# Kernel tuning notes

Hardware: AMD Instinct MI355X
Metric: run time of the kernel (lower is better)

## Reference

```python
import jax, jax.numpy as jnp
import numpy as np

LN_EPS = 1e-5   # torch LayerNorm default
EPS = 1e-8      # slot-attention renorm eps
ITERS = 3


def _ln(x, g, b):
    m = jnp.mean(x, axis=-1, keepdims=True)
    v = jnp.mean(jnp.square(x - m), axis=-1, keepdims=True)
    return (x - m) * jax.lax.rsqrt(v + LN_EPS) * g + b


def _gru(x, h, W_ih, W_hh, b_ih, b_hh):
    # torch GRUCell: gates ordered r, z, n; weight_* has shape [3h, in]
    gi = x @ W_ih.T + b_ih
    gh = h @ W_hh.T + b_hh
    ir, iz, inn = jnp.split(gi, 3, axis=-1)
    hr, hz, hn = jnp.split(gh, 3, axis=-1)
    r = jax.nn.sigmoid(ir + hr)
    z = jax.nn.sigmoid(iz + hz)
    n = jnp.tanh(inn + r * hn)
    return (1.0 - z) * n + z * h


def setup_inputs() -> dict:
    key = jax.random.key(0)
    ks = jax.random.split(key, 16)
    b, n, d, n_s = 32, 4096, 256, 8
    h = max(d, 128)  # hidden_dim = max(dim, hidden_dim)
    s = 1.0 / np.sqrt(d)
    inp = {
        "inputs": jax.random.normal(ks[0], (b, n, d), jnp.float32),
        "noise": jax.random.normal(ks[1], (b, n_s, d), jnp.float32),
        "slots_mu": jax.random.normal(ks[2], (1, 1, d), jnp.float32),
        "slots_logsigma": jax.random.normal(ks[3], (1, 1, d), jnp.float32) * 0.1,
        "Wq": jax.random.uniform(ks[4], (d, d), jnp.float32, -s, s),
        "bq": jnp.zeros((d,), jnp.float32),
        "Wk": jax.random.uniform(ks[5], (d, d), jnp.float32, -s, s),
        "bk": jnp.zeros((d,), jnp.float32),
        "Wv": jax.random.uniform(ks[6], (d, d), jnp.float32, -s, s),
        "bv": jnp.zeros((d,), jnp.float32),
        "W_ih": jax.random.uniform(ks[7], (3 * d, d), jnp.float32, -s, s),
        "W_hh": jax.random.uniform(ks[8], (3 * d, d), jnp.float32, -s, s),
        "b_ih": jnp.zeros((3 * d,), jnp.float32),
        "b_hh": jnp.zeros((3 * d,), jnp.float32),
        "W1": jax.random.uniform(ks[9], (h, d), jnp.float32, -s, s),
        "b1": jnp.zeros((h,), jnp.float32),
        "W2": jax.random.uniform(ks[10], (d, h), jnp.float32, -s, s),
        "b2": jnp.zeros((d,), jnp.float32),
        "g_in": jnp.ones((d,), jnp.float32), "be_in": jnp.zeros((d,), jnp.float32),
        "g_sl": jnp.ones((d,), jnp.float32), "be_sl": jnp.zeros((d,), jnp.float32),
        "g_ff": jnp.ones((d,), jnp.float32), "be_ff": jnp.zeros((d,), jnp.float32),
    }
    return inp


def reference(inputs, noise, slots_mu, slots_logsigma, Wq, bq, Wk, bk, Wv, bv,
              W_ih, W_hh, b_ih, b_hh, W1, b1, W2, b2,
              g_in, be_in, g_sl, be_sl, g_ff, be_ff):
    b, n, d = inputs.shape
    scale = d ** (-0.5)
    # reparameterized slot init
    slots = slots_mu + jnp.exp(slots_logsigma) * noise          # [b, n_s, d]
    x = _ln(inputs, g_in, be_in)
    k = x @ Wk.T + bk                                           # [b, n, d]
    v = x @ Wv.T + bv
    attn = None
    for _ in range(ITERS):
        slots_prev = slots
        q = _ln(slots, g_sl, be_sl) @ Wq.T + bq                 # [b, n_s, d]
        dots = jnp.einsum('bid,bjd->bij', q, k) * scale         # [b, n_s, n]
        attn = jax.nn.softmax(dots, axis=1)                     # softmax over SLOTS
        attn_ = attn + EPS
        attn_ = attn_ / jnp.sum(attn_, axis=-1, keepdims=True)  # renorm over inputs
        updates = jnp.einsum('bjd,bij->bid', v, attn_)          # [b, n_s, d]
        slots = _gru(updates.reshape(-1, d), slots_prev.reshape(-1, d),
                     W_ih, W_hh, b_ih, b_hh).reshape(b, -1, d)
        pre = _ln(slots, g_ff, be_ff)
        slots = slots + (jax.nn.relu(pre @ W1.T + b1) @ W2.T + b2)
    return (slots, attn)
```

## Files before the change

kernel.cpp:

```cpp
#include <hip/hip_runtime.h>
#include <hip/hip_fp16.h>
#include <cstdint>
#include <cstddef>


#define NTOK 4096
#define DDIM 256
#define NSLOT 8
#define NBATCH 32
#define CH 64
#define NCHK 64
#define SROWS (NBATCH * NSLOT)
#define NROWS (NBATCH * NTOK)
#define SCALE 0.0625f
#define LN_EPS_C 1e-5f
#define ATTN_EPS_C 1e-8f

__device__ __forceinline__ void wave_reduce2(float& s, float& ss) {
#pragma unroll
  for (int off = 32; off > 0; off >>= 1) {
    s  += __shfl_down(s, off, 64);
    ss += __shfl_down(ss, off, 64);
  }
}
__device__ __forceinline__ void wave_reduce2_xor(float& s, float& ss) {
#pragma unroll
  for (int off = 32; off > 0; off >>= 1) {
    s  += __shfl_xor(s, off, 64);
    ss += __shfl_xor(ss, off, 64);
  }
}

__global__ __launch_bounds__(256) void convert_weights_k(
    const float* __restrict__ Wq, const float* __restrict__ Wv,
    const float* __restrict__ Wih, const float* __restrict__ Whh,
    const float* __restrict__ W1, const float* __restrict__ W2,
    const float* __restrict__ Wk, __half* __restrict__ WqT,
    __half* __restrict__ WvT, __half* __restrict__ WihT,
    __half* __restrict__ WhhT, __half* __restrict__ W1T,
    __half* __restrict__ W2T, __half* __restrict__ Wk_h) {
  __shared__ float tile[32][33];
  int bz = blockIdx.x;
  int tx = threadIdx.x & 31, ty = threadIdx.x >> 5;
  if (bz >= 80) {
    int ro = (bz - 80) * 32, cd = blockIdx.y * 32;
#pragma unroll
    for (int p = 0; p < 32; p += 8)
      Wk_h[(size_t)(ro + ty + p) * DDIM + cd + tx] =
          __float2half(Wk[(size_t)(ro + ty + p) * DDIM + cd + tx]);
    return;
  }
  const float* in; __half* out; int O, bo;
  if (bz < 8)       { in = Wq;  out = WqT;  O = 256; bo = bz; }
  else if (bz < 16) { in = Wv;  out = WvT;  O = 256; bo = bz - 8; }
  else if (bz < 40) { in = Wih; out = WihT; O = 768; bo = bz - 16; }
  else if (bz < 64) { in = Whh; out = WhhT; O = 768; bo = bz - 40; }
  else if (bz < 72) { in = W1;  out = W1T;  O = 256; bo = bz - 64; }
  else              { in = W2;  out = W2T;  O = 256; bo = bz - 72; }
  int ro = bo * 32, cd = blockIdx.y * 32;
#pragma unroll
  for (int p = 0; p < 32; p += 8)
    tile[ty + p][tx] = in[(size_t)(ro + ty + p) * DDIM + cd + tx];
  __syncthreads();
#pragma unroll
  for (int p = 0; p < 32; p += 8)
    out[(size_t)(cd + ty + p) * O + ro + tx] = __float2half(tile[tx][ty + p]);
}

__global__ __launch_bounds__(256) void xh_prep_k(
    const float* __restrict__ X, const float* __restrict__ g,
    const float* __restrict__ be, __half* __restrict__ xh) {
  int row = blockIdx.x * 4 + (threadIdx.x >> 6);
  int lane = threadIdx.x & 63;
  float4 a = *(const float4*)(X + (size_t)row * DDIM + lane * 4);
  float s = a.x + a.y + a.z + a.w;
  float ss = a.x * a.x + a.y * a.y + a.z * a.z + a.w * a.w;
  wave_reduce2_xor(s, ss);
  float m = s * (1.f / DDIM);
  float rs = rsqrtf(ss * (1.f / DDIM) - m * m + LN_EPS_C);
  float4 gv = *(const float4*)(g + lane * 4);
  float4 bev = *(const float4*)(be + lane * 4);
  union { __half2 h[2]; uint2 u; } pk;
  pk.h[0] = __floats2half2_rn((a.x - m) * rs * gv.x + bev.x,
                              (a.y - m) * rs * gv.y + bev.y);
  pk.h[1] = __floats2half2_rn((a.z - m) * rs * gv.z + bev.z,
                              (a.w - m) * rs * gv.w + bev.w);
  *(uint2*)(xh + (size_t)row * DDIM + lane * 4) = pk.u;
}

__global__ __launch_bounds__(256) void fused_attn_f16_k(
    const __half* __restrict__ xh, const float* __restrict__ qk,
    const float* __restrict__ qkb, float* __restrict__ attn_out,
    float* __restrict__ S_part, __half* __restrict__ u_part, int write_attn) {
  __shared__ __half sx[CH][258];
  __shared__ float4 sq4[NSLOT][64];
  __shared__ float part[4][NSLOT][CH];
  __shared__ float sa[NSLOT][CH];
  __shared__ float sC0[NSLOT], sS[NSLOT];
  int b = blockIdx.x, c = blockIdx.y, t = threadIdx.x;
#pragma unroll
  for (int r2 = 0; r2 < 2; ++r2) {
    int idx = r2 * 256 + t;
    int i = idx >> 6, quad = idx & 63;
    sq4[i][quad] = *(const float4*)(qk + ((size_t)b * NSLOT + i) * DDIM + quad * 4);
  }
  if (t < NSLOT) sC0[t] = qkb[b * NSLOT + t];
  const size_t base = (size_t)b * NTOK + (size_t)c * CH;
#pragma unroll
  for (int it = 0; it < 8; ++it) {
    int e = it * 256 + t;
    int row = e >> 5, c16 = e & 31;
    uint4 v = *(const uint4*)(xh + (base + row) * DDIM + c16 * 8);
    __half2* dst = (__half2*)&sx[row][c16 * 8];
    dst[0] = ((const __half2*)&v)[0];
    dst[1] = ((const __half2*)&v)[1];
    dst[2] = ((const __half2*)&v)[2];
    dst[3] = ((const __half2*)&v)[3];
  }
  __syncthreads();
  {
    int tj = t & 31, qd = t >> 5;
    float2 xa[16], xb[16];
    const __half2* xra = (const __half2*)&sx[tj][qd * 32];
    const __half2* xrb = (const __half2*)&sx[tj + 32][qd * 32];
#pragma unroll
    for (int d2 = 0; d2 < 16; ++d2) {
      xa[d2] = __half22float2(xra[d2]);
      xb[d2] = __half22float2(xrb[d2]);
    }
    int w = t >> 6;
    bool lo = (t & 63) < 32;
#pragma unroll
    for (int i = 0; i < NSLOT; ++i) {
      float pa = 0.f, pb = 0.f;
#pragma unroll
      for (int d4 = 0; d4 < 8; ++d4) {
        float4 q = sq4[i][qd * 8 + d4];
        pa = fmaf(xa[2 * d4].x, q.x, fmaf(xa[2 * d4].y, q.y,
             fmaf(xa[2 * d4 + 1].x, q.z, fmaf(xa[2 * d4 + 1].y, q.w, pa))));
        pb = fmaf(xb[2 * d4].x, q.x, fmaf(xb[2 * d4].y, q.y,
             fmaf(xb[2 * d4 + 1].x, q.z, fmaf(xb[2 * d4 + 1].y, q.w, pb))));
      }
      pa += __shfl_down(pa, 32, 64);
      pb += __shfl_down(pb, 32, 64);
      if (lo) { part[w][i][tj] = pa; part[w][i][tj + 32] = pb; }
    }
  }
  __syncthreads();
  if (t < CH) {
    float dots[NSLOT], mx = -1e30f;
#pragma unroll
    for (int i = 0; i < NSLOT; ++i) {
      dots[i] = part[0][i][t] + part[1][i][t] + part[2][i][t] +
                part[3][i][t] + sC0[i];
      mx = fmaxf(mx, dots[i]);
    }
    float sum = 0.f;
#pragma unroll
    for (int i = 0; i < NSLOT; ++i) { dots[i] = expf(dots[i] - mx); sum += dots[i]; }
    float inv = 1.f / sum;
#pragma unroll
    for (int i = 0; i < NSLOT; ++i) {
      float a = dots[i] * inv;
      if (write_attn)
        attn_out[((size_t)b * NSLOT + i) * NTOK + c * CH + t] = a;
      float ae = a + ATTN_EPS_C;
      sa[i][t] = ae;
      float ps = ae;
#pragma unroll
      for (int off = 32; off > 0; off >>= 1) ps += __shfl_down(ps, off, 64);
      if (t == 0) sS[i] = ps;
    }
  }
  __syncthreads();
  float acc[NSLOT] = {};
#pragma unroll
  for (int jj = 0; jj < CH; ++jj) {
    float x = __half2float(sx[jj][t]);
#pragma unroll
    for (int i = 0; i < NSLOT; ++i) acc[i] = fmaf(x, sa[i][jj], acc[i]);
  }
  __half* upb = u_part + (((size_t)b * NCHK + c) * NSLOT) * DDIM + t;
#pragma unroll
  for (int i = 0; i < NSLOT; ++i) upb[(size_t)i * DDIM] = __float2half(acc[i]);
  if (t < NSLOT) S_part[((size_t)b * NCHK + c) * NSLOT + t] = sS[t];
}

__global__ __launch_bounds__(1024) void slot_update_k(
    const __half* __restrict__ u_part, const float* __restrict__ S_part,
    const float* __restrict__ slots_in, const __half* __restrict__ WvT,
    const float* __restrict__ bv, const __half* __restrict__ WihT,
    const __half* __restrict__ WhhT, const float* __restrict__ b_ih,
    const float* __restrict__ b_hh, const float* __restrict__ g_ff,
    const float* __restrict__ be_ff, const __half* __restrict__ W1T,
    const float* __restrict__ b1, const __half* __restrict__ W2T,
    const float* __restrict__ b2, const float* __restrict__ g_sl,
    const float* __restrict__ be_sl, const __half* __restrict__ WqT,
    const float* __restrict__ bq, const __half* __restrict__ Wk_h,
    const float* __restrict__ bk, const float* __restrict__ noise,
    const float* __restrict__ mu, const float* __restrict__ logsig,
    float* __restrict__ slots_out, float* __restrict__ qk,
    float* __restrict__ qkb_out, int init, int compute_qk) {
  __shared__ float red[4][6][DDIM];
  __shared__ float su[DDIM], sh[DDIM], supd[DDIM], v1[DDIM], v2[DDIM];
  __shared__ float scal[16];
  int r = blockIdx.x, t = threadIdx.x;
  int b = r >> 3, i = r & 7;
  int o = t & 255, ks = t >> 8;
  int lane = t & 63, wid = t >> 6;
  if (init) {
    if (ks == 0) {
      float ns = mu[o] + expf(logsig[o]) * noise[(size_t)r * DDIM + o];
      slots_out[(size_t)r * DDIM + o] = ns;
      v2[o] = ns;
    }
    __syncthreads();
  } else {
    {
      float up = 0.f;
      const __half* upp =
          u_part + (((size_t)b * NCHK + ks * 16) * NSLOT + i) * DDIM + o;
#pragma unroll
      for (int cc = 0; cc < 16; ++cc)
        up += __half2float(upp[(size_t)cc * (NSLOT * DDIM)]);
      red[ks][0][o] = up;
    }
    if (t < 64) {
      float sp = S_part[((size_t)b * NCHK + t) * NSLOT + i];
#pragma unroll
      for (int off = 32; off > 0; off >>= 1) sp += __shfl_down(sp, off, 64);
      if (t == 0) scal[0] = sp;
    }
    if (ks == 0) sh[o] = slots_in[(size_t)r * DDIM + o];
    __syncthreads();
    if (ks == 0) {
      float invS = 1.f / scal[0];
      su[o] = (red[0][0][o] + red[1][0][o] + red[2][0][o] + red[3][0][o]) * invS;
    }
    __syncthreads();
    {
      float p = 0.f;
      const __half* wp = WvT + (size_t)(ks * 64) * DDIM + o;
#pragma unroll 8
      for (int dd = 0; dd < 64; ++dd)
        p = fmaf(su[ks * 64 + dd], __half2float(wp[(size_t)dd * DDIM]), p);
      red[ks][0][o] = p;
    }
    __syncthreads();
    if (ks == 0)
      supd[o] = bv[o] + red[0][0][o] + red[1][0][o] + red[2][0][o] + red[3][0][o];
    __syncthreads();
    {
      float p0 = 0, p1 = 0, p2 = 0, p3 = 0, p4 = 0, p5 = 0;
      const __half* pi = WihT + (size_t)(ks * 64) * (3 * DDIM) + o;
      const __half* ph = WhhT + (size_t)(ks * 64) * (3 * DDIM) + o;
#pragma unroll 4
      for (int dd = 0; dd < 64; ++dd) {
        float ud = supd[ks * 64 + dd], hd = sh[ks * 64 + dd];
        size_t off = (size_t)dd * (3 * DDIM);
        p0 = fmaf(ud, __half2float(pi[off]), p0);
        p1 = fmaf(ud, __half2float(pi[off + DDIM]), p1);
        p2 = fmaf(ud, __half2float(pi[off + 2 * DDIM]), p2);
        p3 = fmaf(hd, __half2float(ph[off]), p3);
        p4 = fmaf(hd, __half2float(ph[off + DDIM]), p4);
        p5 = fmaf(hd, __half2float(ph[off + 2 * DDIM]), p5);
      }
      red[ks][0][o] = p0; red[ks][1][o] = p1; red[ks][2][o] = p2;
      red[ks][3][o] = p3; red[ks][4][o] = p4; red[ks][5][o] = p5;
    }
    __syncthreads();
    if (ks == 0) {
      float air = b_ih[o] + red[0][0][o] + red[1][0][o] + red[2][0][o] + red[3][0][o];
      float aiz = b_ih[DDIM + o] + red[0][1][o] + red[1][1][o] + red[2][1][o] + red[3][1][o];
      float ain = b_ih[2 * DDIM + o] + red[0][2][o] + red[1][2][o] + red[2][2][o] + red[3][2][o];
      float ahr = b_hh[o] + red[0][3][o] + red[1][3][o] + red[2][3][o] + red[3][3][o];
      float ahz = b_hh[DDIM + o] + red[0][4][o] + red[1][4][o] + red[2][4][o] + red[3][4][o];
      float ahn = b_hh[2 * DDIM + o] + red[0][5][o] + red[1][5][o] + red[2][5][o] + red[3][5][o];
      float rg = 1.f / (1.f + expf(-(air + ahr)));
      float zg = 1.f / (1.f + expf(-(aiz + ahz)));
      float ng = tanhf(ain + rg * ahn);
      float nh = (1.f - zg) * ng + zg * sh[o];
      v1[o] = nh;
      float s2 = nh, ss2 = nh * nh;
      wave_reduce2(s2, ss2);
      if (lane == 0) { scal[wid] = s2; scal[4 + wid] = ss2; }
    }
    __syncthreads();
    if (ks == 0) {
      float sS = scal[0] + scal[1] + scal[2] + scal[3];
      float sQ = scal[4] + scal[5] + scal[6] + scal[7];
      float m = sS * (1.f / DDIM);
      float rs = rsqrtf(sQ * (1.f / DDIM) - m * m + LN_EPS_C);
      v2[o] = (v1[o] - m) * rs * g_ff[o] + be_ff[o];
    }
    __syncthreads();
    {
      float p = 0.f;
      const __half* wp = W1T + (size_t)(ks * 64) * DDIM + o;
#pragma unroll 8
      for (int dd = 0; dd < 64; ++dd)
        p = fmaf(v2[ks * 64 + dd], __half2float(wp[(size_t)dd * DDIM]), p);
      red[ks][0][o] = p;
    }
    __syncthreads();
    if (ks == 0)
      su[o] = fmaxf(b1[o] + red[0][0][o] + red[1][0][o] + red[2][0][o] + red[3][0][o], 0.f);
    __syncthreads();
    {
      float p = 0.f;
      const __half* wp = W2T + (size_t)(ks * 64) * DDIM + o;
#pragma unroll 8
      for (int dd = 0; dd < 64; ++dd)
        p = fmaf(su[ks * 64 + dd], __half2float(wp[(size_t)dd * DDIM]), p);
      red[ks][0][o] = p;
    }
    __syncthreads();
    if (ks == 0) {
      float out = v1[o] + b2[o] + red[0][0][o] + red[1][0][o] + red[2][0][o] + red[3][0][o];
      slots_out[(size_t)r * DDIM + o] = out;
      v2[o] = out;
    }
    __syncthreads();
  }
  if (!compute_qk) return;
  if (ks == 0) {
    float x = v2[o];
    float s2 = x, ss2 = x * x;
    wave_reduce2(s2, ss2);
    if (lane == 0) { scal[wid] = s2; scal[4 + wid] = ss2; }
  }
  __syncthreads();
  if (ks == 0) {
    float sS = scal[0] + scal[1] + scal[2] + scal[3];
    float sQ = scal[4] + scal[5] + scal[6] + scal[7];
    float m = sS * (1.f / DDIM);
    float rs = rsqrtf(sQ * (1.f / DDIM) - m * m + LN_EPS_C);
    su[o] = (v2[o] - m) * rs * g_sl[o] + be_sl[o];
  }
  __syncthreads();
  {
    float p = 0.f;
    const __half* wp = WqT + (size_t)(ks * 64) * DDIM + o;
#pragma unroll 8
    for (int dd = 0; dd < 64; ++dd)
      p = fmaf(su[ks * 64 + dd], __half2float(wp[(size_t)dd * DDIM]), p);
    red[ks][0][o] = p;
  }
  __syncthreads();
  if (ks == 0)
    sh[o] = bq[o] + red[0][0][o] + red[1][0][o] + red[2][0][o] + red[3][0][o];
  __syncthreads();
  {
    float p = 0.f;
    const __half* wp = Wk_h + (size_t)(ks * 64) * DDIM + o;
#pragma unroll 8
    for (int dd = 0; dd < 64; ++dd)
      p = fmaf(sh[ks * 64 + dd], __half2float(wp[(size_t)dd * DDIM]), p);
    red[ks][0][o] = p;
  }
  __syncthreads();
  if (ks == 0) {
    float qkv = SCALE * (red[0][0][o] + red[1][0][o] + red[2][0][o] + red[3][0][o]);
    qk[(size_t)r * DDIM + o] = qkv;
    float v0 = sh[o] * bk[o], d1 = 0.f;
    wave_reduce2(v0, d1);
    if (lane == 0) scal[wid] = v0;
  }
  __syncthreads();
  if (t == 0)
    qkb_out[r] = SCALE * (scal[0] + scal[1] + scal[2] + scal[3]);
}

extern "C" void kernel_launch(void* const* d_in, const int* in_sizes, int n_in,
                              void* d_out, int out_size, void* d_ws,
                              size_t ws_size, hipStream_t stream) {
  const float* inputs   = (const float*)d_in[0];
  const float* noise    = (const float*)d_in[1];
  const float* slots_mu = (const float*)d_in[2];
  const float* slots_ls = (const float*)d_in[3];
  const float* Wq   = (const float*)d_in[4];
  const float* bq   = (const float*)d_in[5];
  const float* Wk   = (const float*)d_in[6];
  const float* bk   = (const float*)d_in[7];
  const float* Wv   = (const float*)d_in[8];
  const float* bv   = (const float*)d_in[9];
  const float* W_ih = (const float*)d_in[10];
  const float* W_hh = (const float*)d_in[11];
  const float* b_ih = (const float*)d_in[12];
  const float* b_hh = (const float*)d_in[13];
  const float* W1   = (const float*)d_in[14];
  const float* b1   = (const float*)d_in[15];
  const float* W2   = (const float*)d_in[16];
  const float* b2   = (const float*)d_in[17];
  const float* g_in = (const float*)d_in[18];
  const float* be_in= (const float*)d_in[19];
  const float* g_sl = (const float*)d_in[20];
  const float* be_sl= (const float*)d_in[21];
  const float* g_ff = (const float*)d_in[22];
  const float* be_ff= (const float*)d_in[23];

  float* out_slots = (float*)d_out;
  float* out_attn  = (float*)d_out + SROWS * DDIM;

  float* w = (float*)d_ws;
  float* slots = w;  w += SROWS * DDIM;
  float* qk = w;     w += SROWS * DDIM;
  float* qkb = w;    w += SROWS;
  float* S_part = w; w += NBATCH * NCHK * NSLOT;
  __half* h = (__half*)w;
  __half* xh = h;     h += (size_t)NROWS * DDIM;
  __half* u_part = h; h += (size_t)NBATCH * NCHK * NSLOT * DDIM;
  __half* WqT_h = h;  h += DDIM * DDIM;
  __half* WvT_h = h;  h += DDIM * DDIM;
  __half* WihT_h = h; h += DDIM * 3 * DDIM;
  __half* WhhT_h = h; h += DDIM * 3 * DDIM;
  __half* W1T_h = h;  h += DDIM * DDIM;
  __half* W2T_h = h;  h += DDIM * DDIM;
  __half* Wk_h = h;   h += DDIM * DDIM;

  convert_weights_k<<<dim3(88, 8), 256, 0, stream>>>(
      Wq, Wv, W_ih, W_hh, W1, W2, Wk, WqT_h, WvT_h, WihT_h, WhhT_h, W1T_h,
      W2T_h, Wk_h);
  slot_update_k<<<SROWS, 1024, 0, stream>>>(
      u_part, S_part, slots, WvT_h, bv, WihT_h, WhhT_h, b_ih, b_hh, g_ff,
      be_ff, W1T_h, b1, W2T_h, b2, g_sl, be_sl, WqT_h, bq, Wk_h, bk, noise,
      slots_mu, slots_ls, slots, qk, qkb, 1, 1);
  xh_prep_k<<<NROWS / 4, 256, 0, stream>>>(inputs, g_in, be_in, xh);
  for (int it = 0; it < 3; ++it) {
    fused_attn_f16_k<<<dim3(NBATCH, NCHK), 256, 0, stream>>>(
        xh, qk, qkb, out_attn, S_part, u_part, (it == 2) ? 1 : 0);
    float* sout = (it == 2) ? out_slots : slots;
    slot_update_k<<<SROWS, 1024, 0, stream>>>(
        u_part, S_part, slots, WvT_h, bv, WihT_h, WhhT_h, b_ih, b_hh, g_ff,
        be_ff, W1T_h, b1, W2T_h, b2, g_sl, be_sl, WqT_h, bq, Wk_h, bk, noise,
        slots_mu, slots_ls, sout, qk, qkb, 0, (it == 2) ? 0 : 1);
  }
}
```

Baseline: 240.6 us.

## Double-buffer token chunks via async global-to-LDS loads in fused attention

Each attention block now processes four token chunks instead of one, loading chunks with global_load_lds into two XOR-swizzled LDS buffers so the next chunk's load overlaps the current chunk's compute. The query is stored in LDS as half2, and the renormalised attention reuses the partial-sum buffer. The goal is to hide global load latency, cut LDS bank conflicts and amortise per-block setup. The grid shrinks fourfold, which lowers parallelism, and the hand-placed waitcnt and barrier ordering is fragile.

```diff
diff --git a/kernel.cpp b/kernel.cpp
--- a/kernel.cpp
+++ b/kernel.cpp
@@ -92,98 +92,143 @@
     const __half* __restrict__ xh, const float* __restrict__ qk,
     const float* __restrict__ qkb, float* __restrict__ attn_out,
     float* __restrict__ S_part, __half* __restrict__ u_part, int write_attn) {
-  __shared__ __half sx[CH][258];
-  __shared__ float4 sq4[NSLOT][64];
+  __shared__ __align__(16) char sx[2][CH * 512];
+  __shared__ __half2 sqh[NSLOT][128];
   __shared__ float part[4][NSLOT][CH];
-  __shared__ float sa[NSLOT][CH];
-  __shared__ float sC0[NSLOT], sS[NSLOT];
-  int b = blockIdx.x, c = blockIdx.y, t = threadIdx.x;
-#pragma unroll
-  for (int r2 = 0; r2 < 2; ++r2) {
+#define SA(i, j) part[0][i][j]
+  int b = blockIdx.x, t = threadIdx.x;
+  int c0 = blockIdx.y * 4;
+  int lane = t & 63, w = t >> 6;
+
+#pragma unroll
+  for (int r2 = 0; r2 < 4; ++r2) {
     int idx = r2 * 256 + t;
-    int i = idx >> 6, quad = idx & 63;
-    sq4[i][quad] = *(const float4*)(qk + ((size_t)b * NSLOT + i) * DDIM + quad * 4);
-  }
-  if (t < NSLOT) sC0[t] = qkb[b * NSLOT + t];
-  const size_t base = (size_t)b * NTOK + (size_t)c * CH;
-#pragma unroll
-  for (int it = 0; it < 8; ++it) {
-    int e = it * 256 + t;
-    int row = e >> 5, c16 = e & 31;
-    uint4 v = *(const uint4*)(xh + (base + row) * DDIM + c16 * 8);
-    __half2* dst = (__half2*)&sx[row][c16 * 8];
-    dst[0] = ((const __half2*)&v)[0];
-    dst[1] = ((const __half2*)&v)[1];
-    dst[2] = ((const __half2*)&v)[2];
-    dst[3] = ((const __half2*)&v)[3];
-  }
-  __syncthreads();
-  {
-    int tj = t & 31, qd = t >> 5;
-    float2 xa[16], xb[16];
-    const __half2* xra = (const __half2*)&sx[tj][qd * 32];
-    const __half2* xrb = (const __half2*)&sx[tj + 32][qd * 32];
-#pragma unroll
-    for (int d2 = 0; d2 < 16; ++d2) {
-      xa[d2] = __half22float2(xra[d2]);
-      xb[d2] = __half22float2(xrb[d2]);
-    }
-    int w = t >> 6;
-    bool lo = (t & 63) < 32;
-#pragma unroll
-    for (int i = 0; i < NSLOT; ++i) {
-      float pa = 0.f, pb = 0.f;
-#pragma unroll
-      for (int d4 = 0; d4 < 8; ++d4) {
-        float4 q = sq4[i][qd * 8 + d4];
-        pa = fmaf(xa[2 * d4].x, q.x, fmaf(xa[2 * d4].y, q.y,
-             fmaf(xa[2 * d4 + 1].x, q.z, fmaf(xa[2 * d4 + 1].y, q.w, pa))));
-        pb = fmaf(xb[2 * d4].x, q.x, fmaf(xb[2 * d4].y, q.y,
-             fmaf(xb[2 * d4 + 1].x, q.z, fmaf(xb[2 * d4 + 1].y, q.w, pb))));
-      }
-      pa += __shfl_down(pa, 32, 64);
-      pb += __shfl_down(pb, 32, 64);
-      if (lo) { part[w][i][tj] = pa; part[w][i][tj + 32] = pb; }
-    }
-  }
-  __syncthreads();
-  if (t < CH) {
-    float dots[NSLOT], mx = -1e30f;
-#pragma unroll
-    for (int i = 0; i < NSLOT; ++i) {
-      dots[i] = part[0][i][t] + part[1][i][t] + part[2][i][t] +
-                part[3][i][t] + sC0[i];
-      mx = fmaxf(mx, dots[i]);
-    }
-    float sum = 0.f;
-#pragma unroll
-    for (int i = 0; i < NSLOT; ++i) { dots[i] = expf(dots[i] - mx); sum += dots[i]; }
-    float inv = 1.f / sum;
-#pragma unroll
-    for (int i = 0; i < NSLOT; ++i) {
-      float a = dots[i] * inv;
-      if (write_attn)
-        attn_out[((size_t)b * NSLOT + i) * NTOK + c * CH + t] = a;
-      float ae = a + ATTN_EPS_C;
-      sa[i][t] = ae;
-      float ps = ae;
-#pragma unroll
-      for (int off = 32; off > 0; off >>= 1) ps += __shfl_down(ps, off, 64);
-      if (t == 0) sS[i] = ps;
-    }
-  }
-  __syncthreads();
-  float acc[NSLOT] = {};
-#pragma unroll
-  for (int jj = 0; jj < CH; ++jj) {
-    float x = __half2float(sx[jj][t]);
-#pragma unroll
-    for (int i = 0; i < NSLOT; ++i) acc[i] = fmaf(x, sa[i][jj], acc[i]);
-  }
-  __half* upb = u_part + (((size_t)b * NCHK + c) * NSLOT) * DDIM + t;
-#pragma unroll
-  for (int i = 0; i < NSLOT; ++i) upb[(size_t)i * DDIM] = __float2half(acc[i]);
-  if (t < NSLOT) S_part[((size_t)b * NCHK + c) * NSLOT + t] = sS[t];
+    int i = idx >> 7, d2 = idx & 127;
+    const float* qr = qk + ((size_t)b * NSLOT + i) * DDIM + d2 * 2;
+    sqh[i][d2] = __floats2half2_rn(qr[0], qr[1]);
+  }
+
+  const size_t rowb = (size_t)b * NTOK;
+
+  auto issue = [&](int buf, int chunk) {
+#pragma unroll
+    for (int k = 0; k < 8; ++k) {
+      int seg = w * 8 + k;
+      int L = (seg << 10) + lane * 16;
+      int row = L >> 9, col = L & 511;
+      int scol = col ^ ((row & 15) << 4);
+      const __half* src =
+          xh + (rowb + (size_t)chunk * CH + row) * DDIM + (scol >> 1);
+      __builtin_amdgcn_global_load_lds(
+          (const __attribute__((address_space(1))) void*)src,
+          (__attribute__((address_space(3))) void*)(&sx[buf][seg << 10]),
+          16, 0, 0);
+    }
+  };
+
+  auto compute = [&](int buf, int chunk) {
+    const char* sb = sx[buf];
+    {
+      int tj = t & 31, qd = (t >> 5) & 7;
+      int sw = (tj & 15) << 4;
+      float2 xa[16], xb[16];
+#pragma unroll
+      for (int d2 = 0; d2 < 16; ++d2) {
+        int ca = qd * 64 + d2 * 4;
+        xa[d2] = __half22float2(*(const __half2*)(sb + tj * 512 + (ca ^ sw)));
+        xb[d2] =
+            __half22float2(*(const __half2*)(sb + (tj + 32) * 512 + (ca ^ sw)));
+      }
+      bool lo = (t & 63) < 32;
+#pragma unroll
+      for (int i = 0; i < NSLOT; ++i) {
+        float pa = 0.f, pb = 0.f;
+#pragma unroll
+        for (int d2 = 0; d2 < 16; ++d2) {
+          float2 qf = __half22float2(sqh[i][qd * 16 + d2]);
+          pa = fmaf(xa[d2].x, qf.x, fmaf(xa[d2].y, qf.y, pa));
+          pb = fmaf(xb[d2].x, qf.x, fmaf(xb[d2].y, qf.y, pb));
+        }
+        pa += __shfl_down(pa, 32, 64);
+        pb += __shfl_down(pb, 32, 64);
+        if (lo) { part[w][i][tj] = pa; part[w][i][tj + 32] = pb; }
+      }
+    }
+    asm volatile("s_waitcnt lgkmcnt(0)" ::: "memory");
+    __builtin_amdgcn_s_barrier();
+    if (t < CH) {
+      float dots[NSLOT], mx = -1e30f;
+#pragma unroll
+      for (int i = 0; i < NSLOT; ++i) {
+        dots[i] = part[0][i][t] + part[1][i][t] + part[2][i][t] +
+                  part[3][i][t] + qkb[b * NSLOT + i];
+        mx = fmaxf(mx, dots[i]);
+      }
+      float sum = 0.f;
+#pragma unroll
+      for (int i = 0; i < NSLOT; ++i) {
+        dots[i] = expf(dots[i] - mx);
+        sum += dots[i];
+      }
+      float inv = 1.f / sum;
+#pragma unroll
+      for (int i = 0; i < NSLOT; ++i) {
+        float a = dots[i] * inv;
+        if (write_attn)
+          attn_out[((size_t)b * NSLOT + i) * NTOK + chunk * CH + t] = a;
+        dots[i] = a + ATTN_EPS_C;
+      }
+#pragma unroll
+      for (int i = 0; i < NSLOT; ++i) {
+        float ps = dots[i];
+#pragma unroll
+        for (int off = 32; off > 0; off >>= 1) ps += __shfl_down(ps, off, 64);
+        if (t == 0) S_part[((size_t)b * NCHK + chunk) * NSLOT + i] = ps;
+      }
+#pragma unroll
+      for (int i = 0; i < NSLOT; ++i) SA(i, t) = dots[i];
+    }
+    asm volatile("s_waitcnt lgkmcnt(0)" ::: "memory");
+    __builtin_amdgcn_s_barrier();
+    {
+      float acc[NSLOT] = {};
+#pragma unroll 8
+      for (int jj = 0; jj < CH; ++jj) {
+        int ad = jj * 512 + ((2 * t) ^ ((jj & 15) << 4));
+        float x = __half2float(*(const __half*)(sb + ad));
+#pragma unroll
+        for (int i = 0; i < NSLOT; ++i) acc[i] = fmaf(x, SA(i, jj), acc[i]);
+      }
+      __half* upb = u_part + (((size_t)b * NCHK + chunk) * NSLOT) * DDIM + t;
+#pragma unroll
+      for (int i = 0; i < NSLOT; ++i)
+        upb[(size_t)i * DDIM] = __float2half(acc[i]);
+    }
+  };
+
+  issue(0, c0);
+  issue(1, c0 + 1);
+  asm volatile("s_waitcnt vmcnt(8) lgkmcnt(0)" ::: "memory");
+  __builtin_amdgcn_s_barrier();
+  compute(0, c0);
+  asm volatile("s_waitcnt lgkmcnt(0)" ::: "memory");
+  __builtin_amdgcn_s_barrier();
+  issue(0, c0 + 2);
+  asm volatile("s_waitcnt vmcnt(8)" ::: "memory");
+  __builtin_amdgcn_s_barrier();
+  compute(1, c0 + 1);
+  asm volatile("s_waitcnt lgkmcnt(0)" ::: "memory");
+  __builtin_amdgcn_s_barrier();
+  issue(1, c0 + 3);
+  asm volatile("s_waitcnt vmcnt(8)" ::: "memory");
+  __builtin_amdgcn_s_barrier();
+  compute(0, c0 + 2);
+  asm volatile("s_waitcnt lgkmcnt(0)" ::: "memory");
+  __builtin_amdgcn_s_barrier();
+  asm volatile("s_waitcnt vmcnt(0)" ::: "memory");
+  __builtin_amdgcn_s_barrier();
+  compute(1, c0 + 3);
+#undef SA
 }
 
 __global__ __launch_bounds__(1024) void slot_update_k(
@@ -427,7 +472,7 @@
       slots_mu, slots_ls, slots, qk, qkb, 1, 1);
   xh_prep_k<<<NROWS / 4, 256, 0, stream>>>(inputs, g_in, be_in, xh);
   for (int it = 0; it < 3; ++it) {
-    fused_attn_f16_k<<<dim3(NBATCH, NCHK), 256, 0, stream>>>(
+    fused_attn_f16_k<<<dim3(NBATCH, 16), 256, 0, stream>>>(
         xh, qk, qkb, out_attn, S_part, u_part, (it == 2) ? 1 : 0);
     float* sout = (it == 2) ? out_slots : slots;
     slot_update_k<<<SROWS, 1024, 0, stream>>>(
```

Result: slower. 280.4 us (+16.6%).

## Split fused attention into packed-f16 dot/softmax kernel and separate update kernel

Applied to the files above, without the earlier changes.

Replaces the single fused attention kernel with two kernels. The first computes slot dots with packed f16 `fdot2` against register-resident q, does the softmax over slots, writes eps-shifted attention weights to global memory as half, and emits per-chunk sums. The second rereads xh to accumulate weighted updates over 256-token chunks and writes the attn output from the stored half weights. This drops the shared-memory staging and cross-wave reductions, at the cost of reading xh twice per iteration and storing the final attention at reduced precision.

```diff
diff --git a/kernel.cpp b/kernel.cpp
--- a/kernel.cpp
+++ b/kernel.cpp
@@ -8,13 +8,19 @@
 #define DDIM 256
 #define NSLOT 8
 #define NBATCH 32
-#define CH 64
-#define NCHK 64
 #define SROWS (NBATCH * NSLOT)
 #define NROWS (NBATCH * NTOK)
 #define SCALE 0.0625f
 #define LN_EPS_C 1e-5f
 #define ATTN_EPS_C 1e-8f
+
+typedef _Float16 f16x2 __attribute__((ext_vector_type(2)));
+
+__device__ __forceinline__ f16x2 u2h(unsigned u) {
+  union { unsigned u; f16x2 h; } c;
+  c.u = u;
+  return c.h;
+}
 
 __device__ __forceinline__ void wave_reduce2(float& s, float& ss) {
 #pragma unroll
@@ -88,102 +94,115 @@
   *(uint2*)(xh + (size_t)row * DDIM + lane * 4) = pk.u;
 }
 
-__global__ __launch_bounds__(256) void fused_attn_f16_k(
+__global__ __launch_bounds__(256) void dots_k(
     const __half* __restrict__ xh, const float* __restrict__ qk,
-    const float* __restrict__ qkb, float* __restrict__ attn_out,
-    float* __restrict__ S_part, __half* __restrict__ u_part, int write_attn) {
-  __shared__ __half sx[CH][258];
-  __shared__ float4 sq4[NSLOT][64];
-  __shared__ float part[4][NSLOT][CH];
-  __shared__ float sa[NSLOT][CH];
-  __shared__ float sC0[NSLOT], sS[NSLOT];
-  int b = blockIdx.x, c = blockIdx.y, t = threadIdx.x;
-#pragma unroll
-  for (int r2 = 0; r2 < 2; ++r2) {
-    int idx = r2 * 256 + t;
-    int i = idx >> 6, quad = idx & 63;
-    sq4[i][quad] = *(const float4*)(qk + ((size_t)b * NSLOT + i) * DDIM + quad * 4);
-  }
-  if (t < NSLOT) sC0[t] = qkb[b * NSLOT + t];
-  const size_t base = (size_t)b * NTOK + (size_t)c * CH;
-#pragma unroll
+    const float* __restrict__ qkb, __half* __restrict__ ae_g,
+    float* __restrict__ S_part) {
+  __shared__ float red[4][8];
+  int b = blockIdx.x, g = blockIdx.y, t = threadIdx.x;
+  int w = t >> 6, lane = t & 63;
+  int sub = lane >> 4, r = lane & 15;
+  f16x2 qk2[NSLOT][8];
+#pragma unroll
+  for (int i = 0; i < NSLOT; ++i) {
+    const float* qr = qk + ((size_t)b * NSLOT + i) * DDIM + r * 16;
+#pragma unroll
+    for (int d4 = 0; d4 < 4; ++d4) {
+      float4 q4 = *(const float4*)(qr + d4 * 4);
+      qk2[i][d4 * 2] = (f16x2){(_Float16)q4.x, (_Float16)q4.y};
+      qk2[i][d4 * 2 + 1] = (f16x2){(_Float16)q4.z, (_Float16)q4.w};
+    }
+  }
+  float qkb_r[NSLOT];
+#pragma unroll
+  for (int i = 0; i < NSLOT; ++i) qkb_r[i] = qkb[b * NSLOT + i];
+  float sacc = 0.f;
+  const size_t tokbase = (size_t)b * NTOK + (size_t)g * 128;
   for (int it = 0; it < 8; ++it) {
-    int e = it * 256 + t;
-    int row = e >> 5, c16 = e & 31;
-    uint4 v = *(const uint4*)(xh + (base + row) * DDIM + c16 * 8);
-    __half2* dst = (__half2*)&sx[row][c16 * 8];
-    dst[0] = ((const __half2*)&v)[0];
-    dst[1] = ((const __half2*)&v)[1];
-    dst[2] = ((const __half2*)&v)[2];
-    dst[3] = ((const __half2*)&v)[3];
-  }
-  __syncthreads();
-  {
-    int tj = t & 31, qd = t >> 5;
-    float2 xa[16], xb[16];
-    const __half2* xra = (const __half2*)&sx[tj][qd * 32];
-    const __half2* xrb = (const __half2*)&sx[tj + 32][qd * 32];
-#pragma unroll
-    for (int d2 = 0; d2 < 16; ++d2) {
-      xa[d2] = __half22float2(xra[d2]);
-      xb[d2] = __half22float2(xrb[d2]);
-    }
-    int w = t >> 6;
-    bool lo = (t & 63) < 32;
+    int tok = it * 16 + w * 4 + sub;
+    const __half* xr = xh + (tokbase + tok) * DDIM + r * 16;
+    uint4 v0 = *(const uint4*)(xr);
+    uint4 v1 = *(const uint4*)(xr + 8);
+    f16x2 x2[8];
+    x2[0] = u2h(v0.x); x2[1] = u2h(v0.y); x2[2] = u2h(v0.z); x2[3] = u2h(v0.w);
+    x2[4] = u2h(v1.x); x2[5] = u2h(v1.y); x2[6] = u2h(v1.z); x2[7] = u2h(v1.w);
+    float p[NSLOT];
 #pragma unroll
     for (int i = 0; i < NSLOT; ++i) {
-      float pa = 0.f, pb = 0.f;
-#pragma unroll
-      for (int d4 = 0; d4 < 8; ++d4) {
-        float4 q = sq4[i][qd * 8 + d4];
-        pa = fmaf(xa[2 * d4].x, q.x, fmaf(xa[2 * d4].y, q.y,
-             fmaf(xa[2 * d4 + 1].x, q.z, fmaf(xa[2 * d4 + 1].y, q.w, pa))));
-        pb = fmaf(xb[2 * d4].x, q.x, fmaf(xb[2 * d4].y, q.y,
-             fmaf(xb[2 * d4 + 1].x, q.z, fmaf(xb[2 * d4 + 1].y, q.w, pb))));
-      }
-      pa += __shfl_down(pa, 32, 64);
-      pb += __shfl_down(pb, 32, 64);
-      if (lo) { part[w][i][tj] = pa; part[w][i][tj + 32] = pb; }
-    }
-  }
-  __syncthreads();
-  if (t < CH) {
-    float dots[NSLOT], mx = -1e30f;
+      float s = 0.f;
+#pragma unroll
+      for (int d2 = 0; d2 < 8; ++d2)
+        s = __builtin_amdgcn_fdot2(x2[d2], qk2[i][d2], s, false);
+      p[i] = s;
+    }
 #pragma unroll
     for (int i = 0; i < NSLOT; ++i) {
-      dots[i] = part[0][i][t] + part[1][i][t] + part[2][i][t] +
-                part[3][i][t] + sC0[i];
-      mx = fmaxf(mx, dots[i]);
-    }
+      p[i] += __shfl_xor(p[i], 1, 64);
+      p[i] += __shfl_xor(p[i], 2, 64);
+      p[i] += __shfl_xor(p[i], 4, 64);
+      p[i] += __shfl_xor(p[i], 8, 64);
+      p[i] += qkb_r[i];
+    }
+    float mx = -1e30f;
+#pragma unroll
+    for (int i = 0; i < NSLOT; ++i) mx = fmaxf(mx, p[i]);
     float sum = 0.f;
 #pragma unroll
-    for (int i = 0; i < NSLOT; ++i) { dots[i] = expf(dots[i] - mx); sum += dots[i]; }
+    for (int i = 0; i < NSLOT; ++i) { p[i] = expf(p[i] - mx); sum += p[i]; }
     float inv = 1.f / sum;
-#pragma unroll
-    for (int i = 0; i < NSLOT; ++i) {
-      float a = dots[i] * inv;
-      if (write_attn)
-        attn_out[((size_t)b * NSLOT + i) * NTOK + c * CH + t] = a;
-      float ae = a + ATTN_EPS_C;
-      sa[i][t] = ae;
-      float ps = ae;
-#pragma unroll
-      for (int off = 32; off > 0; off >>= 1) ps += __shfl_down(ps, off, 64);
-      if (t == 0) sS[i] = ps;
-    }
-  }
+    if (r < NSLOT) {
+      float ae = p[r] * inv + ATTN_EPS_C;
+      ae_g[(tokbase + tok) * NSLOT + r] = __float2half(ae);
+      sacc += ae;
+    }
+  }
+  sacc += __shfl_down(sacc, 32, 64);
+  sacc += __shfl_down(sacc, 16, 64);
+  if (lane < NSLOT) red[w][lane] = sacc;
+  __syncthreads();
+  if (t < NSLOT) {
+    float s = red[0][t] + red[1][t] + red[2][t] + red[3][t];
+    S_part[((size_t)b * 32 + g) * NSLOT + t] = s;
+  }
+}
+
+__global__ __launch_bounds__(256) void update_k(
+    const __half* __restrict__ xh, const __half* __restrict__ ae_g,
+    float* __restrict__ attn_out, __half* __restrict__ u_part,
+    int write_attn) {
+  __shared__ __align__(16) __half sa[256 * NSLOT];
+  int b = blockIdx.x, g = blockIdx.y, t = threadIdx.x;
+  const size_t tokbase = (size_t)b * NTOK + (size_t)g * 256;
+  *(uint4*)&sa[t * 8] = *(const uint4*)(ae_g + tokbase * NSLOT + t * 8);
   __syncthreads();
   float acc[NSLOT] = {};
-#pragma unroll
-  for (int jj = 0; jj < CH; ++jj) {
-    float x = __half2float(sx[jj][t]);
-#pragma unroll
-    for (int i = 0; i < NSLOT; ++i) acc[i] = fmaf(x, sa[i][jj], acc[i]);
-  }
-  __half* upb = u_part + (((size_t)b * NCHK + c) * NSLOT) * DDIM + t;
+  const __half* xb = xh + tokbase * DDIM + t;
+#pragma unroll 8
+  for (int jj = 0; jj < 256; ++jj) {
+    float x = __half2float(xb[(size_t)jj * DDIM]);
+    const __half2* a2 = (const __half2*)&sa[jj * 8];
+    float2 f0 = __half22float2(a2[0]);
+    float2 f1 = __half22float2(a2[1]);
+    float2 f2 = __half22float2(a2[2]);
+    float2 f3 = __half22float2(a2[3]);
+    acc[0] = fmaf(x, f0.x, acc[0]);
+    acc[1] = fmaf(x, f0.y, acc[1]);
+    acc[2] = fmaf(x, f1.x, acc[2]);
+    acc[3] = fmaf(x, f1.y, acc[3]);
+    acc[4] = fmaf(x, f2.x, acc[4]);
+    acc[5] = fmaf(x, f2.y, acc[5]);
+    acc[6] = fmaf(x, f3.x, acc[6]);
+    acc[7] = fmaf(x, f3.y, acc[7]);
+  }
+  __half* upb = u_part + (((size_t)b * 16 + g) * NSLOT) * DDIM + t;
 #pragma unroll
   for (int i = 0; i < NSLOT; ++i) upb[(size_t)i * DDIM] = __float2half(acc[i]);
-  if (t < NSLOT) S_part[((size_t)b * NCHK + c) * NSLOT + t] = sS[t];
+  if (write_attn) {
+#pragma unroll
+    for (int i = 0; i < NSLOT; ++i)
+      attn_out[((size_t)b * NSLOT + i) * NTOK + g * 256 + t] =
+          __half2float(sa[t * 8 + i]) - ATTN_EPS_C;
+  }
 }
 
 __global__ __launch_bounds__(1024) void slot_update_k(
@@ -219,16 +238,16 @@
     {
       float up = 0.f;
       const __half* upp =
-          u_part + (((size_t)b * NCHK + ks * 16) * NSLOT + i) * DDIM + o;
-#pragma unroll
-      for (int cc = 0; cc < 16; ++cc)
+          u_part + (((size_t)b * 16 + ks * 4) * NSLOT + i) * DDIM + o;
+#pragma unroll
+      for (int cc = 0; cc < 4; ++cc)
         up += __half2float(upp[(size_t)cc * (NSLOT * DDIM)]);
       red[ks][0][o] = up;
     }
     if (t < 64) {
-      float sp = S_part[((size_t)b * NCHK + t) * NSLOT + i];
-#pragma unroll
-      for (int off = 32; off > 0; off >>= 1) sp += __shfl_down(sp, off, 64);
+      float sp = (t < 32) ? S_part[((size_t)b * 32 + t) * NSLOT + i] : 0.f;
+#pragma unroll
+      for (int off = 16; off > 0; off >>= 1) sp += __shfl_down(sp, off, 64);
       if (t == 0) scal[0] = sp;
     }
     if (ks == 0) sh[o] = slots_in[(size_t)r * DDIM + o];
@@ -406,10 +425,11 @@
   float* slots = w;  w += SROWS * DDIM;
   float* qk = w;     w += SROWS * DDIM;
   float* qkb = w;    w += SROWS;
-  float* S_part = w; w += NBATCH * NCHK * NSLOT;
+  float* S_part = w; w += NBATCH * 32 * NSLOT;
   __half* h = (__half*)w;
   __half* xh = h;     h += (size_t)NROWS * DDIM;
-  __half* u_part = h; h += (size_t)NBATCH * NCHK * NSLOT * DDIM;
+  __half* u_part = h; h += (size_t)NBATCH * 16 * NSLOT * DDIM;
+  __half* ae_g = h;   h += (size_t)NROWS * NSLOT;
   __half* WqT_h = h;  h += DDIM * DDIM;
   __half* WvT_h = h;  h += DDIM * DDIM;
   __half* WihT_h = h; h += DDIM * 3 * DDIM;
@@ -427,8 +447,9 @@
       slots_mu, slots_ls, slots, qk, qkb, 1, 1);
   xh_prep_k<<<NROWS / 4, 256, 0, stream>>>(inputs, g_in, be_in, xh);
   for (int it = 0; it < 3; ++it) {
-    fused_attn_f16_k<<<dim3(NBATCH, NCHK), 256, 0, stream>>>(
-        xh, qk, qkb, out_attn, S_part, u_part, (it == 2) ? 1 : 0);
+    dots_k<<<dim3(NBATCH, 32), 256, 0, stream>>>(xh, qk, qkb, ae_g, S_part);
+    update_k<<<dim3(NBATCH, 16), 256, 0, stream>>>(
+        xh, ae_g, out_attn, u_part, (it == 2) ? 1 : 0);
     float* sout = (it == 2) ? out_slots : slots;
     slot_update_k<<<SROWS, 1024, 0, stream>>>(
         u_part, S_part, slots, WvT_h, bv, WihT_h, WhhT_h, b_ih, b_hh, g_ff,
```

Measured after the change: 270.1 us. 12.3% more time.

## Restructure attention kernel to per-wave register streaming with fdot2 and deferred attn transpose

Applied to the files above, without the earlier changes.

The shared-memory tiled attention kernel is replaced by a wave-per-64-token design. Each half-wave streams one token per step straight from global memory, computes slot dots with packed fp16 dot2 instructions and cross-lane shuffles, and accumulates slot updates in registers, so the LDS staging and block barriers go away. Partial updates are now stored in fp32. The final attention map is written as a compact fp16 token-major buffer, and a separate kernel transposes it to the output afterwards. The trade-offs are heavy register pressure (64 accumulators per thread), fewer blocks per launch, and fp16 rounding of q and of the attention output, which could hurt accuracy.

```diff
diff --git a/kernel.cpp b/kernel.cpp
--- a/kernel.cpp
+++ b/kernel.cpp
@@ -8,13 +8,15 @@
 #define DDIM 256
 #define NSLOT 8
 #define NBATCH 32
-#define CH 64
-#define NCHK 64
+#define NWV 64
 #define SROWS (NBATCH * NSLOT)
 #define NROWS (NBATCH * NTOK)
 #define SCALE 0.0625f
 #define LN_EPS_C 1e-5f
 #define ATTN_EPS_C 1e-8f
+
+typedef _Float16 f16x2 __attribute__((ext_vector_type(2)));
+union U2H { unsigned u; f16x2 h; __half2 hh; };
 
 __device__ __forceinline__ void wave_reduce2(float& s, float& ss) {
 #pragma unroll
@@ -88,106 +90,126 @@
   *(uint2*)(xh + (size_t)row * DDIM + lane * 4) = pk.u;
 }
 
-__global__ __launch_bounds__(256) void fused_attn_f16_k(
+__global__ __launch_bounds__(256) void fused_k(
     const __half* __restrict__ xh, const float* __restrict__ qk,
-    const float* __restrict__ qkb, float* __restrict__ attn_out,
-    float* __restrict__ S_part, __half* __restrict__ u_part, int write_attn) {
-  __shared__ __half sx[CH][258];
-  __shared__ float4 sq4[NSLOT][64];
-  __shared__ float part[4][NSLOT][CH];
-  __shared__ float sa[NSLOT][CH];
-  __shared__ float sC0[NSLOT], sS[NSLOT];
-  int b = blockIdx.x, c = blockIdx.y, t = threadIdx.x;
-#pragma unroll
-  for (int r2 = 0; r2 < 2; ++r2) {
-    int idx = r2 * 256 + t;
-    int i = idx >> 6, quad = idx & 63;
-    sq4[i][quad] = *(const float4*)(qk + ((size_t)b * NSLOT + i) * DDIM + quad * 4);
-  }
-  if (t < NSLOT) sC0[t] = qkb[b * NSLOT + t];
-  const size_t base = (size_t)b * NTOK + (size_t)c * CH;
-#pragma unroll
-  for (int it = 0; it < 8; ++it) {
-    int e = it * 256 + t;
-    int row = e >> 5, c16 = e & 31;
-    uint4 v = *(const uint4*)(xh + (base + row) * DDIM + c16 * 8);
-    __half2* dst = (__half2*)&sx[row][c16 * 8];
-    dst[0] = ((const __half2*)&v)[0];
-    dst[1] = ((const __half2*)&v)[1];
-    dst[2] = ((const __half2*)&v)[2];
-    dst[3] = ((const __half2*)&v)[3];
-  }
-  __syncthreads();
-  {
-    int tj = t & 31, qd = t >> 5;
-    float2 xa[16], xb[16];
-    const __half2* xra = (const __half2*)&sx[tj][qd * 32];
-    const __half2* xrb = (const __half2*)&sx[tj + 32][qd * 32];
-#pragma unroll
-    for (int d2 = 0; d2 < 16; ++d2) {
-      xa[d2] = __half22float2(xra[d2]);
-      xb[d2] = __half22float2(xrb[d2]);
-    }
-    int w = t >> 6;
-    bool lo = (t & 63) < 32;
+    const float* __restrict__ qkb, float* __restrict__ u_part,
+    float* __restrict__ S_part, __half* __restrict__ ae_buf, int write_ae) {
+  int b = blockIdx.x, t = threadIdx.x;
+  int wv = blockIdx.y * 4 + (t >> 6);
+  int lane = t & 63, half = lane >> 5, r = lane & 31;
+  f16x2 qk2[NSLOT][4];
+#pragma unroll
+  for (int i = 0; i < NSLOT; ++i) {
+    const float* qr = qk + ((size_t)b * NSLOT + i) * DDIM + r * 8;
+    float4 a = *(const float4*)qr;
+    float4 c = *(const float4*)(qr + 4);
+    qk2[i][0] = (f16x2){(_Float16)a.x, (_Float16)a.y};
+    qk2[i][1] = (f16x2){(_Float16)a.z, (_Float16)a.w};
+    qk2[i][2] = (f16x2){(_Float16)c.x, (_Float16)c.y};
+    qk2[i][3] = (f16x2){(_Float16)c.z, (_Float16)c.w};
+  }
+  float qkb_r[NSLOT];
+#pragma unroll
+  for (int i = 0; i < NSLOT; ++i) qkb_r[i] = qkb[b * NSLOT + i];
+  float uacc[NSLOT][8] = {};
+  float sacc[NSLOT] = {};
+  const __half* base = xh + ((size_t)b * NTOK + (size_t)wv * 64) * DDIM;
+#pragma unroll 4
+  for (int p = 0; p < 32; ++p) {
+    int tok = p * 2 + half;
+    uint4 v = *(const uint4*)(base + (size_t)tok * DDIM + r * 8);
+    U2H x0, x1, x2, x3;
+    x0.u = v.x; x1.u = v.y; x2.u = v.z; x3.u = v.w;
+    float dot[NSLOT];
 #pragma unroll
     for (int i = 0; i < NSLOT; ++i) {
-      float pa = 0.f, pb = 0.f;
-#pragma unroll
-      for (int d4 = 0; d4 < 8; ++d4) {
-        float4 q = sq4[i][qd * 8 + d4];
-        pa = fmaf(xa[2 * d4].x, q.x, fmaf(xa[2 * d4].y, q.y,
-             fmaf(xa[2 * d4 + 1].x, q.z, fmaf(xa[2 * d4 + 1].y, q.w, pa))));
-        pb = fmaf(xb[2 * d4].x, q.x, fmaf(xb[2 * d4].y, q.y,
-             fmaf(xb[2 * d4 + 1].x, q.z, fmaf(xb[2 * d4 + 1].y, q.w, pb))));
-      }
-      pa += __shfl_down(pa, 32, 64);
-      pb += __shfl_down(pb, 32, 64);
-      if (lo) { part[w][i][tj] = pa; part[w][i][tj + 32] = pb; }
-    }
-  }
-  __syncthreads();
-  if (t < CH) {
-    float dots[NSLOT], mx = -1e30f;
+      float s = 0.f;
+      s = __builtin_amdgcn_fdot2(x0.h, qk2[i][0], s, false);
+      s = __builtin_amdgcn_fdot2(x1.h, qk2[i][1], s, false);
+      s = __builtin_amdgcn_fdot2(x2.h, qk2[i][2], s, false);
+      s = __builtin_amdgcn_fdot2(x3.h, qk2[i][3], s, false);
+      dot[i] = s;
+    }
 #pragma unroll
     for (int i = 0; i < NSLOT; ++i) {
-      dots[i] = part[0][i][t] + part[1][i][t] + part[2][i][t] +
-                part[3][i][t] + sC0[i];
-      mx = fmaxf(mx, dots[i]);
-    }
+      dot[i] += __shfl_xor(dot[i], 1, 64);
+      dot[i] += __shfl_xor(dot[i], 2, 64);
+      dot[i] += __shfl_xor(dot[i], 4, 64);
+      dot[i] += __shfl_xor(dot[i], 8, 64);
+      dot[i] += __shfl_xor(dot[i], 16, 64);
+      dot[i] += qkb_r[i];
+    }
+    float mx = dot[0];
+#pragma unroll
+    for (int i = 1; i < NSLOT; ++i) mx = fmaxf(mx, dot[i]);
     float sum = 0.f;
-#pragma unroll
-    for (int i = 0; i < NSLOT; ++i) { dots[i] = expf(dots[i] - mx); sum += dots[i]; }
+    float ae[NSLOT];
+#pragma unroll
+    for (int i = 0; i < NSLOT; ++i) { ae[i] = __expf(dot[i] - mx); sum += ae[i]; }
     float inv = 1.f / sum;
 #pragma unroll
     for (int i = 0; i < NSLOT; ++i) {
-      float a = dots[i] * inv;
-      if (write_attn)
-        attn_out[((size_t)b * NSLOT + i) * NTOK + c * CH + t] = a;
-      float ae = a + ATTN_EPS_C;
-      sa[i][t] = ae;
-      float ps = ae;
-#pragma unroll
-      for (int off = 32; off > 0; off >>= 1) ps += __shfl_down(ps, off, 64);
-      if (t == 0) sS[i] = ps;
-    }
-  }
-  __syncthreads();
-  float acc[NSLOT] = {};
-#pragma unroll
-  for (int jj = 0; jj < CH; ++jj) {
-    float x = __half2float(sx[jj][t]);
-#pragma unroll
-    for (int i = 0; i < NSLOT; ++i) acc[i] = fmaf(x, sa[i][jj], acc[i]);
-  }
-  __half* upb = u_part + (((size_t)b * NCHK + c) * NSLOT) * DDIM + t;
-#pragma unroll
-  for (int i = 0; i < NSLOT; ++i) upb[(size_t)i * DDIM] = __float2half(acc[i]);
-  if (t < NSLOT) S_part[((size_t)b * NCHK + c) * NSLOT + t] = sS[t];
+      ae[i] = fmaf(ae[i], inv, ATTN_EPS_C);
+      sacc[i] += ae[i];
+    }
+    float2 f0 = __half22float2(x0.hh);
+    float2 f1 = __half22float2(x1.hh);
+    float2 f2 = __half22float2(x2.hh);
+    float2 f3 = __half22float2(x3.hh);
+    float xf[8] = {f0.x, f0.y, f1.x, f1.y, f2.x, f2.y, f3.x, f3.y};
+#pragma unroll
+    for (int i = 0; i < NSLOT; ++i)
+#pragma unroll
+      for (int d = 0; d < 8; ++d)
+        uacc[i][d] = fmaf(ae[i], xf[d], uacc[i][d]);
+    if (write_ae && r == 0) {
+      union { __half2 h[4]; uint4 u; } pk;
+#pragma unroll
+      for (int i = 0; i < 4; ++i)
+        pk.h[i] = __floats2half2_rn(ae[2 * i], ae[2 * i + 1]);
+      *(uint4*)(ae_buf + ((size_t)b * NTOK + wv * 64 + tok) * NSLOT) = pk.u;
+    }
+  }
+#pragma unroll
+  for (int i = 0; i < NSLOT; ++i)
+#pragma unroll
+    for (int d = 0; d < 8; ++d)
+      uacc[i][d] += __shfl_down(uacc[i][d], 32, 64);
+  if (half == 0) {
+    float* up = u_part + (((size_t)b * NWV + wv) * NSLOT) * DDIM + r * 8;
+#pragma unroll
+    for (int i = 0; i < NSLOT; ++i) {
+      float4 v0 = {uacc[i][0], uacc[i][1], uacc[i][2], uacc[i][3]};
+      float4 v1 = {uacc[i][4], uacc[i][5], uacc[i][6], uacc[i][7]};
+      *(float4*)(up + (size_t)i * DDIM) = v0;
+      *(float4*)(up + (size_t)i * DDIM + 4) = v1;
+    }
+  }
+#pragma unroll
+  for (int i = 0; i < NSLOT; ++i) sacc[i] += __shfl_down(sacc[i], 32, 64);
+  if (lane == 0) {
+#pragma unroll
+    for (int i = 0; i < NSLOT; ++i)
+      S_part[((size_t)b * NWV + wv) * NSLOT + i] = sacc[i];
+  }
+}
+
+__global__ __launch_bounds__(256) void attn_tr_k(
+    const __half* __restrict__ ae_buf, float* __restrict__ attn) {
+  int b = blockIdx.x;
+  int tok = blockIdx.y * 256 + threadIdx.x;
+  uint4 v = *(const uint4*)(ae_buf + ((size_t)b * NTOK + tok) * NSLOT);
+  const __half2* h = (const __half2*)&v;
+#pragma unroll
+  for (int i = 0; i < 4; ++i) {
+    float2 f = __half22float2(h[i]);
+    attn[((size_t)b * NSLOT + 2 * i) * NTOK + tok] = f.x - ATTN_EPS_C;
+    attn[((size_t)b * NSLOT + 2 * i + 1) * NTOK + tok] = f.y - ATTN_EPS_C;
+  }
 }
 
 __global__ __launch_bounds__(1024) void slot_update_k(
-    const __half* __restrict__ u_part, const float* __restrict__ S_part,
+    const float* __restrict__ u_part, const float* __restrict__ S_part,
     const float* __restrict__ slots_in, const __half* __restrict__ WvT,
     const float* __restrict__ bv, const __half* __restrict__ WihT,
     const __half* __restrict__ WhhT, const float* __restrict__ b_ih,
@@ -218,15 +240,15 @@
   } else {
     {
       float up = 0.f;
-      const __half* upp =
-          u_part + (((size_t)b * NCHK + ks * 16) * NSLOT + i) * DDIM + o;
+      const float* upp =
+          u_part + (((size_t)b * NWV + ks * 16) * NSLOT + i) * DDIM + o;
 #pragma unroll
       for (int cc = 0; cc < 16; ++cc)
-        up += __half2float(upp[(size_t)cc * (NSLOT * DDIM)]);
+        up += upp[(size_t)cc * (NSLOT * DDIM)];
       red[ks][0][o] = up;
     }
     if (t < 64) {
-      float sp = S_part[((size_t)b * NCHK + t) * NSLOT + i];
+      float sp = S_part[((size_t)b * NWV + t) * NSLOT + i];
 #pragma unroll
       for (int off = 32; off > 0; off >>= 1) sp += __shfl_down(sp, off, 64);
       if (t == 0) scal[0] = sp;
@@ -406,10 +428,11 @@
   float* slots = w;  w += SROWS * DDIM;
   float* qk = w;     w += SROWS * DDIM;
   float* qkb = w;    w += SROWS;
-  float* S_part = w; w += NBATCH * NCHK * NSLOT;
+  float* S_part = w; w += NBATCH * NWV * NSLOT;
+  float* u_part = w; w += (size_t)NBATCH * NWV * NSLOT * DDIM;
   __half* h = (__half*)w;
   __half* xh = h;     h += (size_t)NROWS * DDIM;
-  __half* u_part = h; h += (size_t)NBATCH * NCHK * NSLOT * DDIM;
+  __half* ae_buf = h; h += (size_t)NROWS * NSLOT;
   __half* WqT_h = h;  h += DDIM * DDIM;
   __half* WvT_h = h;  h += DDIM * DDIM;
   __half* WihT_h = h; h += DDIM * 3 * DDIM;
@@ -427,12 +450,13 @@
       slots_mu, slots_ls, slots, qk, qkb, 1, 1);
   xh_prep_k<<<NROWS / 4, 256, 0, stream>>>(inputs, g_in, be_in, xh);
   for (int it = 0; it < 3; ++it) {
-    fused_attn_f16_k<<<dim3(NBATCH, NCHK), 256, 0, stream>>>(
-        xh, qk, qkb, out_attn, S_part, u_part, (it == 2) ? 1 : 0);
+    fused_k<<<dim3(NBATCH, 16), 256, 0, stream>>>(
+        xh, qk, qkb, u_part, S_part, ae_buf, (it == 2) ? 1 : 0);
     float* sout = (it == 2) ? out_slots : slots;
     slot_update_k<<<SROWS, 1024, 0, stream>>>(
         u_part, S_part, slots, WvT_h, bv, WihT_h, WhhT_h, b_ih, b_hh, g_ff,
         be_ff, W1T_h, b1, W2T_h, b2, g_sl, be_sl, WqT_h, bq, Wk_h, bk, noise,
         slots_mu, slots_ls, sout, qk, qkb, 0, (it == 2) ? 0 : 1);
   }
-}
+  attn_tr_k<<<dim3(NBATCH, 16), 256, 0, stream>>>(ae_buf, out_attn);
+}
```

After: 275.2 us. 14.4% more time.
